# Kernel optimization log

Measured on AMD Instinct MI355X. Metric: run time of the kernel, lower is better.

The kernel has to match this reference:

```python
import jax, jax.numpy as jnp
import numpy as np

L1, L2, N, C = 4096, 4096, 8, 3


def setup_inputs() -> dict:
    key = jax.random.key(0)
    k1, k2 = jax.random.split(key)
    coords1 = jax.random.uniform(k1, (L1, N, C), dtype=jnp.float32)
    coords2 = jax.random.uniform(k2, (L2, N, C), dtype=jnp.float32)
    return {"coords1": coords1, "coords2": coords2}


def reference(coords1, coords2):
    # coords1: [L1, N, C], coords2: [L2, N, C]
    l1, n, c = coords1.shape
    l2 = coords2.shape[0]
    # Batch-first layout, matching flatten_batch semantics (per-batch NN only)
    q = jnp.swapaxes(coords2, 0, 1)  # [N, L2, C] query points
    r = jnp.swapaxes(coords1, 0, 1)  # [N, L1, C] reference points
    # Squared euclidean distances per batch: [N, L2, L1]
    d2 = (
        jnp.sum(q * q, axis=-1)[:, :, None]
        + jnp.sum(r * r, axis=-1)[:, None, :]
        - 2.0 * jnp.einsum("nlc,nmc->nlm", q, r)
    )
    # tc.nearest returns global flat index; original does fmod(L1) to get the
    # per-batch index — argmin within each batch gives that directly.
    nearest = jnp.argmin(d2, axis=-1)  # [N, L2]
    clusters = nearest.T  # [L2, N]
    # torch.meshgrid(arange(L2), arange(N)) with 'ij' indexing; indices[-1] is
    # the batch index broadcast to [L2, N].
    batch_idx = jnp.broadcast_to(jnp.arange(n, dtype=jnp.int64 if False else jnp.int32), (l2, n))
    return (clusters.reshape(-1), batch_idx.reshape(-1))
```

## Files before the change

### kernel.cpp

```cpp
#include <hip/hip_runtime.h>
#include <float.h>


constexpr int kL1 = 4096, kL2 = 4096, kN = 8;
constexpr int kChunk = 2048;
constexpr int kQPerBlock = 32;
constexpr int kQ = 4;

__global__ __launch_bounds__(256, 4)
void nearest_kernel(const float* __restrict__ c1, const float* __restrict__ c2,
                    int* __restrict__ out) {
#pragma clang fp contract(off)
  __shared__ float4 refs[kChunk];

  const int tid = threadIdx.x;
  const int n = blockIdx.y;

  const int g = tid >> 5;
  const int lane = tid & 31;
  const int q0 = blockIdx.x * kQPerBlock + g * kQ;

  float qx[kQ], qy[kQ], qz[kQ], qq[kQ];
#pragma unroll
  for (int i = 0; i < kQ; ++i) {
    const float* p = c2 + ((q0 + i) * kN + n) * 3;
    qx[i] = p[0]; qy[i] = p[1]; qz[i] = p[2];
    qq[i] = __fadd_rn(__fadd_rn(__fmul_rn(qx[i], qx[i]), __fmul_rn(qy[i], qy[i])),
                      __fmul_rn(qz[i], qz[i]));
  }

  float bdA[kQ], bdB[kQ];
  int tA[kQ], tB[kQ];
#pragma unroll
  for (int i = 0; i < kQ; ++i) { bdA[i] = FLT_MAX; bdB[i] = FLT_MAX; tA[i] = 0; tB[i] = 0; }

  int tglob = 0;
  for (int chunk = 0; chunk < kL1 / kChunk; ++chunk) {
    __syncthreads();

#pragma unroll
    for (int k = 0; k < kChunk / 256; ++k) {
      const int j = tid + 256 * k;
      const float* p = c1 + ((chunk * kChunk + j) * kN + n) * 3;
      const float r0 = p[0], r1 = p[1], r2 = p[2];
      const float rr = __fadd_rn(
          __fadd_rn(__fmul_rn(r0, r0), __fmul_rn(r1, r1)), __fmul_rn(r2, r2));
      refs[j] = make_float4(r0, r1, r2, rr);
    }
    __syncthreads();

#pragma unroll 2
    for (int t2 = 0; t2 < kChunk / 64; ++t2, ++tglob) {
      const float4 rA = refs[t2 * 64 + lane];
      const float4 rB = refs[t2 * 64 + lane + 32];
#pragma unroll
      for (int i = 0; i < kQ; ++i) {
        const float dotA = __fadd_rn(
            __fadd_rn(__fmul_rn(qx[i], rA.x), __fmul_rn(qy[i], rA.y)),
            __fmul_rn(qz[i], rA.z));
        const float dA = __fmaf_rn(-2.0f, dotA, __fadd_rn(qq[i], rA.w));
        if (dA < bdA[i]) { bdA[i] = dA; tA[i] = tglob; }

        const float dotB = __fadd_rn(
            __fadd_rn(__fmul_rn(qx[i], rB.x), __fmul_rn(qy[i], rB.y)),
            __fmul_rn(qz[i], rB.z));
        const float dB = __fmaf_rn(-2.0f, dotB, __fadd_rn(qq[i], rB.w));
        if (dB < bdB[i]) { bdB[i] = dB; tB[i] = tglob; }
      }
    }
  }

  float bd[kQ]; int bj[kQ];
#pragma unroll
  for (int i = 0; i < kQ; ++i) {
    const int jA = tA[i] * 64 + lane;
    const int jB = tB[i] * 64 + lane + 32;
    bd[i] = bdA[i]; bj[i] = jA;
    if (bdB[i] < bd[i] || (bdB[i] == bd[i] && jB < bj[i])) { bd[i] = bdB[i]; bj[i] = jB; }
  }

#pragma unroll
  for (int m = 1; m <= 16; m <<= 1) {
#pragma unroll
    for (int i = 0; i < kQ; ++i) {
      const float od = __shfl_xor(bd[i], m);
      const int oj = __shfl_xor(bj[i], m);
      if (od < bd[i] || (od == bd[i] && oj < bj[i])) { bd[i] = od; bj[i] = oj; }
    }
  }

  if (lane == 0) {
#pragma unroll
    for (int i = 0; i < kQ; ++i) {
      out[(q0 + i) * kN + n] = bj[i];
      out[kL2 * kN + (q0 + i) * kN + n] = n;
    }
  }
}

extern "C" void kernel_launch(void* const* d_in, const int* in_sizes, int n_in,
                              void* d_out, int out_size, void* d_ws, size_t ws_size,
                              hipStream_t stream) {
  const float* c1 = (const float*)d_in[0];
  const float* c2 = (const float*)d_in[1];
  int* out = (int*)d_out;
  dim3 grid(kL2 / kQPerBlock, kN);
  nearest_kernel<<<grid, dim3(256), 0, stream>>>(c1, c2, out);
}
```

Baseline: 93.61 us.

## Use full 64-lane waves with packed v2f distance math and smaller blocks

Moves from 32-lane groups to full 64-lane wavefronts, so each wave handles 4 queries and each lane scans one reference per step, and the final reduction grows to 6 shuffle levels. The distance arithmetic is packed into 2-wide float vectors so the compiler can emit packed FP32 instructions (v_pk_mul/add/fma) that work on two queries at once. Block size drops to 16 queries with a 1024-entry LDS chunk and launch bounds of 8 blocks per CU, which raises occupancy. In exchange, each block reloads the reference set for fewer queries, and the extra shuffle level adds reduction work.

```diff
diff --git a/kernel.cpp b/kernel.cpp
--- a/kernel.cpp
+++ b/kernel.cpp
@@ -2,12 +2,14 @@
 #include <float.h>
 
 
+typedef float v2f __attribute__((ext_vector_type(2)));
+
 constexpr int kL1 = 4096, kL2 = 4096, kN = 8;
-constexpr int kChunk = 2048;
-constexpr int kQPerBlock = 32;
+constexpr int kChunk = 1024;
+constexpr int kQPerBlock = 16;
 constexpr int kQ = 4;
 
-__global__ __launch_bounds__(256, 4)
+__global__ __launch_bounds__(256, 8)
 void nearest_kernel(const float* __restrict__ c1, const float* __restrict__ c2,
                     int* __restrict__ out) {
 #pragma clang fp contract(off)
@@ -15,26 +17,30 @@
 
   const int tid = threadIdx.x;
   const int n = blockIdx.y;
+  const int wave = tid >> 6;
+  const int lane = tid & 63;
+  const int q0 = blockIdx.x * kQPerBlock + wave * kQ;
 
-  const int g = tid >> 5;
-  const int lane = tid & 31;
-  const int q0 = blockIdx.x * kQPerBlock + g * kQ;
-
-  float qx[kQ], qy[kQ], qz[kQ], qq[kQ];
+  float qx[kQ], qy[kQ], qz[kQ], qqv[kQ];
 #pragma unroll
   for (int i = 0; i < kQ; ++i) {
     const float* p = c2 + ((q0 + i) * kN + n) * 3;
     qx[i] = p[0]; qy[i] = p[1]; qz[i] = p[2];
-    qq[i] = __fadd_rn(__fadd_rn(__fmul_rn(qx[i], qx[i]), __fmul_rn(qy[i], qy[i])),
-                      __fmul_rn(qz[i], qz[i]));
+    qqv[i] = __fadd_rn(__fadd_rn(__fmul_rn(qx[i], qx[i]), __fmul_rn(qy[i], qy[i])),
+                       __fmul_rn(qz[i], qz[i]));
   }
+  const v2f qx01 = {qx[0], qx[1]}, qx23 = {qx[2], qx[3]};
+  const v2f qy01 = {qy[0], qy[1]}, qy23 = {qy[2], qy[3]};
+  const v2f qz01 = {qz[0], qz[1]}, qz23 = {qz[2], qz[3]};
+  const v2f qq01 = {qqv[0], qqv[1]}, qq23 = {qqv[2], qqv[3]};
 
-  float bdA[kQ], bdB[kQ];
-  int tA[kQ], tB[kQ];
+  float bd[kQ];
+  int bi[kQ];
 #pragma unroll
-  for (int i = 0; i < kQ; ++i) { bdA[i] = FLT_MAX; bdB[i] = FLT_MAX; tA[i] = 0; tB[i] = 0; }
+  for (int i = 0; i < kQ; ++i) { bd[i] = FLT_MAX; bi[i] = 0; }
 
-  int tglob = 0;
+  int jcur = lane;
+
   for (int chunk = 0; chunk < kL1 / kChunk; ++chunk) {
     __syncthreads();
 
@@ -50,49 +56,53 @@
     __syncthreads();
 
 #pragma unroll 2
-    for (int t2 = 0; t2 < kChunk / 64; ++t2, ++tglob) {
-      const float4 rA = refs[t2 * 64 + lane];
-      const float4 rB = refs[t2 * 64 + lane + 32];
-#pragma unroll
-      for (int i = 0; i < kQ; ++i) {
-        const float dotA = __fadd_rn(
-            __fadd_rn(__fmul_rn(qx[i], rA.x), __fmul_rn(qy[i], rA.y)),
-            __fmul_rn(qz[i], rA.z));
-        const float dA = __fmaf_rn(-2.0f, dotA, __fadd_rn(qq[i], rA.w));
-        if (dA < bdA[i]) { bdA[i] = dA; tA[i] = tglob; }
+    for (int t = 0; t < kChunk / 64; ++t) {
+      const float4 r = refs[t * 64 + lane];
+      const v2f rx = {r.x, r.x};
+      const v2f ry = {r.y, r.y};
+      const v2f rz = {r.z, r.z};
+      const v2f rw = {r.w, r.w};
 
-        const float dotB = __fadd_rn(
-            __fadd_rn(__fmul_rn(qx[i], rB.x), __fmul_rn(qy[i], rB.y)),
-            __fmul_rn(qz[i], rB.z));
-        const float dB = __fmaf_rn(-2.0f, dotB, __fadd_rn(qq[i], rB.w));
-        if (dB < bdB[i]) { bdB[i] = dB; tB[i] = tglob; }
+      {
+        const v2f m0 = qx01 * rx;
+        const v2f m1 = qy01 * ry;
+        const v2f s01 = m0 + m1;
+        const v2f m2 = qz01 * rz;
+        const v2f dot = s01 + m2;
+        const v2f A = qq01 + rw;
+        const v2f d = __builtin_elementwise_fma((v2f){-2.0f, -2.0f}, dot, A);
+        if (d.x < bd[0]) { bd[0] = d.x; bi[0] = jcur; }
+        if (d.y < bd[1]) { bd[1] = d.y; bi[1] = jcur; }
       }
+      {
+        const v2f m0 = qx23 * rx;
+        const v2f m1 = qy23 * ry;
+        const v2f s01 = m0 + m1;
+        const v2f m2 = qz23 * rz;
+        const v2f dot = s01 + m2;
+        const v2f A = qq23 + rw;
+        const v2f d = __builtin_elementwise_fma((v2f){-2.0f, -2.0f}, dot, A);
+        if (d.x < bd[2]) { bd[2] = d.x; bi[2] = jcur; }
+        if (d.y < bd[3]) { bd[3] = d.y; bi[3] = jcur; }
+      }
+      jcur += 64;
     }
   }
 
-  float bd[kQ]; int bj[kQ];
 #pragma unroll
-  for (int i = 0; i < kQ; ++i) {
-    const int jA = tA[i] * 64 + lane;
-    const int jB = tB[i] * 64 + lane + 32;
-    bd[i] = bdA[i]; bj[i] = jA;
-    if (bdB[i] < bd[i] || (bdB[i] == bd[i] && jB < bj[i])) { bd[i] = bdB[i]; bj[i] = jB; }
-  }
-
-#pragma unroll
-  for (int m = 1; m <= 16; m <<= 1) {
+  for (int m = 1; m <= 32; m <<= 1) {
 #pragma unroll
     for (int i = 0; i < kQ; ++i) {
       const float od = __shfl_xor(bd[i], m);
-      const int oj = __shfl_xor(bj[i], m);
-      if (od < bd[i] || (od == bd[i] && oj < bj[i])) { bd[i] = od; bj[i] = oj; }
+      const int oj = __shfl_xor(bi[i], m);
+      if (od < bd[i] || (od == bd[i] && oj < bi[i])) { bd[i] = od; bi[i] = oj; }
     }
   }
 
   if (lane == 0) {
 #pragma unroll
     for (int i = 0; i < kQ; ++i) {
-      out[(q0 + i) * kN + n] = bj[i];
+      out[(q0 + i) * kN + n] = bi[i];
       out[kL2 * kN + (q0 + i) * kN + n] = n;
     }
   }
```

Result: faster. 90.18 us (-3.7%).
